# Kernel tuning notes

Hardware: AMD Instinct MI355X
Metric: run time of the kernel (lower is better)

The kernel has to match this reference:

```python
import jax, jax.numpy as jnp
import numpy as np

LN_EPS = 1e-12


def setup_inputs() -> dict:
    key = jax.random.key(0)
    ks = jax.random.split(key, 10)
    B, S, W, D, H = 16, 512, 5, 200, 768
    std = 0.02
    return {
        "layer_output": jax.random.normal(ks[0], (B, S, H), dtype=jnp.float32),
        "word_embeddings": jax.random.normal(ks[1], (B, S, W, D), dtype=jnp.float32),
        "word_mask": jax.random.randint(ks[2], (B, S, W), 0, 2, dtype=jnp.int64),
        "W1": jax.random.normal(ks[3], (D, H), dtype=jnp.float32) * std,
        "b1": jnp.zeros((H,), dtype=jnp.float32),
        "W2": jax.random.normal(ks[4], (H, H), dtype=jnp.float32) * std,
        "b2": jnp.zeros((H,), dtype=jnp.float32),
        "attn_W": jax.random.normal(ks[5], (H, H), dtype=jnp.float32) * std,
        "ln_gamma": jnp.ones((H,), dtype=jnp.float32),
        "ln_beta": jnp.zeros((H,), dtype=jnp.float32),
    }


def reference(layer_output, word_embeddings, word_mask, W1, b1, W2, b2, attn_W, ln_gamma, ln_beta):
    # word_transform: Linear -> Tanh -> Linear (dropout = identity in eval)
    we = jnp.tanh(jnp.einsum("bswd,dh->bswh", word_embeddings, W1) + b1)
    we = jnp.einsum("bswh,hk->bswk", we, W2) + b2  # [B,S,W,H]

    # bilinear word attention: (x @ attn_W) . word_outputs -> score over W
    q = jnp.einsum("bsh,hk->bsk", layer_output, attn_W)  # [B,S,H]
    alpha = jnp.einsum("bsk,bswk->bsw", q, we)            # [B,S,W]
    alpha = alpha + (1.0 - word_mask.astype(alpha.dtype)) * -10000.0
    alpha = jax.nn.softmax(alpha, axis=-1)

    # weighted sum over words + residual
    agg = jnp.einsum("bsw,bswh->bsh", alpha, we)
    h = layer_output + agg

    # LayerNorm (fuse_layer; dropout = identity in eval)
    mu = jnp.mean(h, axis=-1, keepdims=True)
    var = jnp.mean(jnp.square(h - mu), axis=-1, keepdims=True)
    return (h - mu) * jax.lax.rsqrt(var + LN_EPS) * ln_gamma + ln_beta
```

## Files before the change

### kernel.cpp

```cpp
#include <hip/hip_runtime.h>
#include <hip/hip_bf16.h>
#include <math.h>


typedef __attribute__((ext_vector_type(8))) short bf16x8;
typedef __attribute__((ext_vector_type(4))) float f32x4;

__device__ __forceinline__ unsigned short f2bf_bits(float f) {
    __hip_bfloat16 h = __float2bfloat16(f);
    return *reinterpret_cast<unsigned short*>(&h);
}
__device__ __forceinline__ float bf_bits2f(unsigned short u) {
    union { unsigned int i; float f; } v; v.i = ((unsigned int)u) << 16; return v.f;
}
__device__ __forceinline__ float tanh_fast(float x) {
    float xc = fminf(fmaxf(x, -9.f), 9.f);
    float t  = __expf(2.f * xc);
    return (t - 1.f) * __builtin_amdgcn_rcpf(t + 1.f);
}
__device__ __forceinline__ bf16x8 pack8(float4 a, float4 b) {
    union { bf16x8 v; unsigned short s[8]; } u;
    u.s[0]=f2bf_bits(a.x); u.s[1]=f2bf_bits(a.y); u.s[2]=f2bf_bits(a.z); u.s[3]=f2bf_bits(a.w);
    u.s[4]=f2bf_bits(b.x); u.s[5]=f2bf_bits(b.y); u.s[6]=f2bf_bits(b.z); u.s[7]=f2bf_bits(b.w);
    return u.v;
}

__device__ __forceinline__ void async_cp16(const void* g, void* lds) {
#if __has_builtin(__builtin_amdgcn_global_load_lds)
    auto gp = (const __attribute__((address_space(1))) unsigned int*)g;
    auto lp = (__attribute__((address_space(3))) unsigned int*)lds;
    __builtin_amdgcn_global_load_lds(gp, lp, 16, 0, 0);
#else
    *(uint4*)lds = *(const uint4*)g;
#endif
}

__device__ __forceinline__ void sched_fence()  { asm volatile("" ::: "memory"); }
__device__ __forceinline__ void wait8_barrier(){ asm volatile("s_waitcnt vmcnt(8)\ns_barrier" ::: "memory"); }
__device__ __forceinline__ void wait0_barrier(){ asm volatile("s_waitcnt vmcnt(0)\ns_barrier" ::: "memory"); }
__device__ __forceinline__ void barrier_only() { asm volatile("s_barrier" ::: "memory"); }

template<bool F32SRC, bool HAS_BIAS, bool TANH_ACT, bool RESID, bool OUT_BF16,
         int N, int K, int KREAL>
__device__ __forceinline__ void gemm_body(
    const void* __restrict__ Ap, const void* __restrict__ Btp,
    const float* __restrict__ bias, const float* __restrict__ resid,
    void* __restrict__ outp, int m0, int n0, unsigned char* smem)
{
    constexpr int NIT = K / 64;
    const int tid  = threadIdx.x;
    const int lane = tid & 63;
    const int wave = tid >> 6;
    const int wm   = wave & 1;
    const int wn   = wave >> 1;
    const int row16 = lane & 15;
    const int kq    = lane >> 4;

    f32x4 acc[4][4];
#pragma unroll
    for (int i = 0; i < 4; i++)
#pragma unroll
        for (int j = 0; j < 4; j++) acc[i][j] = (f32x4){0.f, 0.f, 0.f, 0.f};

    auto compute_tile = [&](const unsigned short* As, const unsigned short* Bs, bool full) {
        bf16x8 af[2][4], bg[2][4];
#pragma unroll
        for (int mi = 0; mi < 4; mi++) {
            const int r = wm * 64 + mi * 16 + row16;
            af[0][mi] = *(const bf16x8*)&As[r * 64 + (kq ^ (r & 7)) * 8];
            if (full) af[1][mi] = *(const bf16x8*)&As[r * 64 + ((4 + kq) ^ (r & 7)) * 8];
        }
#pragma unroll
        for (int ni = 0; ni < 4; ni++) {
            const int r = wn * 64 + ni * 16 + row16;
            bg[0][ni] = *(const bf16x8*)&Bs[r * 64 + (kq ^ (r & 7)) * 8];
            if (full) bg[1][ni] = *(const bf16x8*)&Bs[r * 64 + ((4 + kq) ^ (r & 7)) * 8];
        }
        __builtin_amdgcn_s_setprio(1);
#pragma unroll
        for (int mi = 0; mi < 4; mi++)
#pragma unroll
            for (int ni = 0; ni < 4; ni++)
                acc[mi][ni] = __builtin_amdgcn_mfma_f32_16x16x32_bf16(
                    af[0][mi], bg[0][ni], acc[mi][ni], 0, 0, 0);
        if (full) {
#pragma unroll
            for (int mi = 0; mi < 4; mi++)
#pragma unroll
                for (int ni = 0; ni < 4; ni++)
                    acc[mi][ni] = __builtin_amdgcn_mfma_f32_16x16x32_bf16(
                        af[1][mi], bg[1][ni], acc[mi][ni], 0, 0, 0);
        }
        __builtin_amdgcn_s_setprio(0);
    };

    if constexpr (F32SRC) {
        const float* A32 = (const float*)Ap;
        const float* B32 = (const float*)Btp;
        unsigned short* As = (unsigned short*)smem;
        unsigned short* Bs = As + 8192;
        for (int t = 0; t < NIT; ++t) {
#pragma unroll
            for (int i = 0; i < 4; ++i) {
                const int c = i * 256 + tid;
                const int row = c >> 3, sl = c & 7;
                const int kcc = sl ^ (row & 7);
                const float* sa = A32 + (size_t)(m0 + row) * K + t * 64 + kcc * 8;
                *(bf16x8*)&As[row * 64 + sl * 8] = pack8(*(const float4*)sa, *(const float4*)(sa + 4));
                const float* sb = B32 + (size_t)(n0 + row) * K + t * 64 + kcc * 8;
                *(bf16x8*)&Bs[row * 64 + sl * 8] = pack8(*(const float4*)sb, *(const float4*)(sb + 4));
            }
            __syncthreads();
            compute_tile(As, Bs, true);
            __syncthreads();
        }
    } else {
        const __hip_bfloat16* A  = (const __hip_bfloat16*)Ap;
        const __hip_bfloat16* Bt = (const __hip_bfloat16*)Btp;
        const int rsub = lane >> 3;
        const int slot = lane & 7;
        const int kc   = slot ^ rsub;
        const __hip_bfloat16* gA = A  + (size_t)(m0 + wave * 32 + rsub) * K + kc * 8;
        const __hip_bfloat16* gB = Bt + (size_t)(n0 + wave * 32 + rsub) * K + kc * 8;
        unsigned short* lA0 = (unsigned short*)smem + wave * 2048 + lane * 8;
        unsigned short* lB0 = lA0 + 8192;

        auto stage = [&](int t, int buf) {
            unsigned short* lA = lA0 + buf * 16384;
            unsigned short* lB = lB0 + buf * 16384;
            const __hip_bfloat16* a = gA + t * 64;
            const __hip_bfloat16* b = gB + t * 64;
#pragma unroll
            for (int i = 0; i < 4; i++) {
                async_cp16(a + (size_t)(8 * i) * K, lA + i * 512);
                async_cp16(b + (size_t)(8 * i) * K, lB + i * 512);
            }
            sched_fence();
        };

        stage(0, 0);
        if (NIT > 1) stage(1, 1);
#pragma unroll
        for (int t = 0; t < NIT; ++t) {
            if (t == NIT - 1) wait0_barrier(); else wait8_barrier();
            const unsigned short* As = (const unsigned short*)(smem + (t & 1) * 32768);
            const unsigned short* Bs = As + 8192;
            compute_tile(As, Bs, (t * 64 + 32 < KREAL));
            barrier_only();
            if (t + 2 < NIT) stage(t + 2, t & 1);
        }
    }

    if (OUT_BF16) {
        unsigned short* rep = (unsigned short*)smem;
#pragma unroll
        for (int ni = 0; ni < 4; ni++) {
            const int c = wn * 64 + ni * 16 + row16;
            float bcol = HAS_BIAS ? bias[n0 + c] : 0.f;
#pragma unroll
            for (int mi = 0; mi < 4; mi++)
#pragma unroll
                for (int r = 0; r < 4; r++) {
                    const int rr = wm * 64 + mi * 16 + kq * 4 + r;
                    float v = acc[mi][ni][r];
                    if (HAS_BIAS) v += bcol;
                    if (TANH_ACT) v = tanh_fast(v);
                    rep[rr * 132 + c] = f2bf_bits(v);
                }
        }
        __syncthreads();
#pragma unroll
        for (int p = 0; p < 8; p++) {
            const int lin = p * 256 + tid;
            const int row = lin >> 4;
            const int c8  = lin & 15;
            const unsigned short* s = &rep[row * 132 + c8 * 8];
            union { uint4 u; unsigned long long q[2]; } d;
            d.q[0] = *(const unsigned long long*)(s);
            d.q[1] = *(const unsigned long long*)(s + 4);
            *(uint4*)((__hip_bfloat16*)outp + (size_t)(m0 + row) * N + n0 + c8 * 8) = d.u;
        }
    } else {
        float* rep = (float*)smem;
#pragma unroll
        for (int h = 0; h < 2; h++) {
            if (wm == h) {
#pragma unroll
                for (int ni = 0; ni < 4; ni++) {
                    const int c = wn * 64 + ni * 16 + row16;
                    float bcol = HAS_BIAS ? bias[n0 + c] : 0.f;
#pragma unroll
                    for (int mi = 0; mi < 4; mi++)
#pragma unroll
                        for (int r = 0; r < 4; r++) {
                            const int rr = mi * 16 + kq * 4 + r;
                            float v = acc[mi][ni][r];
                            if (HAS_BIAS) v += bcol;
                            if (TANH_ACT) v = tanh_fast(v);
                            rep[rr * 132 + c] = v;
                        }
                }
            }
            __syncthreads();
#pragma unroll
            for (int p = 0; p < 8; p++) {
                const int lin = p * 256 + tid;
                const int row = lin >> 5;
                const int c4  = lin & 31;
                float4 v = *(const float4*)&rep[row * 132 + c4 * 4];
                const int grow = m0 + h * 64 + row;
                if (RESID) {
                    float4 rv = *(const float4*)&resid[(size_t)grow * N + n0 + c4 * 4];
                    v.x += rv.x; v.y += rv.y; v.z += rv.z; v.w += rv.w;
                }
                *(float4*)((float*)outp + (size_t)grow * N + n0 + c4 * 4) = v;
            }
            __syncthreads();
        }
    }
}

template<bool HAS_BIAS, bool TANH_ACT, bool RESID, bool OUT_BF16, int N, int K, int GX>
__global__ __launch_bounds__(256) void mfma_gemm(
    const __hip_bfloat16* __restrict__ A,
    const __hip_bfloat16* __restrict__ Bt,
    const float* __restrict__ bias,
    const float* __restrict__ resid,
    void* __restrict__ outp)
{
    __shared__ __align__(16) unsigned char smem[65536];
    int bx, by;
    {
        const int total = gridDim.x;
        const int per_xcd = total >> 3;
        if ((total & 7) == 0 && (per_xcd % GX) == 0) {
            int xcd = blockIdx.x & 7, idx = blockIdx.x >> 3;
            int lin = xcd * per_xcd + idx;
            by = lin / GX; bx = lin % GX;
        } else { by = blockIdx.x / GX; bx = blockIdx.x % GX; }
    }
    gemm_body<false, HAS_BIAS, TANH_ACT, RESID, OUT_BF16, N, K, K>(
        A, Bt, bias, resid, outp, by * 128, bx * 128, smem);
}

__global__ __launch_bounds__(256) void tgemm_kernel(
    const __hip_bfloat16* __restrict__ Eb,
    const __hip_bfloat16* __restrict__ W1Tb,
    const float* __restrict__ b1,
    __hip_bfloat16* __restrict__ Tb)
{
    __shared__ __align__(16) unsigned char smem[65536];
    const int xcd = blockIdx.x & 7, idx = blockIdx.x >> 3;
    const int lin = xcd * 240 + idx;
    gemm_body<false, true, true, false, true, 768, 256, 224>(
        Eb, W1Tb, b1, nullptr, Tb, (lin / 6) * 128, (lin % 6) * 128, smem);
}

__global__ __launch_bounds__(256) void prep_kernel(
    const float* __restrict__ x,  __hip_bfloat16* __restrict__ xb,
    const float* __restrict__ w2,
    const float* __restrict__ aw,
    const float* __restrict__ E,  __hip_bfloat16* __restrict__ Eb,
    const float* __restrict__ W1, __hip_bfloat16* __restrict__ W1Tb,
    __hip_bfloat16* __restrict__ W2Tb,
    __hip_bfloat16* __restrict__ Ctb)
{
    __shared__ __align__(16) unsigned char smem[33792];
    float (*tile)[33] = (float(*)[33])smem;
    const int b = blockIdx.x, tid = threadIdx.x;
    if (b < 36) {
        gemm_body<true, false, false, false, true, 768, 768, 768>(
            w2, aw, nullptr, nullptr, Ctb, (b / 6) * 128, (b % 6) * 128, smem);
    } else if (b < 804) {
        const float* in; __hip_bfloat16* outb; int R, C, Rpad, t;
        if (b < 228) { t = b - 36;  in = W1; outb = W1Tb; R = 200; C = 768; Rpad = 256; }
        else         { t = b - 228; in = w2; outb = W2Tb; R = 768; C = 768; Rpad = 768; }
        const int c0 = (t % 24) * 32, r0 = (t / 24) * 32;
        const int xx = tid & 31, yy = tid >> 5;
#pragma unroll
        for (int i = 0; i < 32; i += 8) {
            int r = r0 + yy + i;
            tile[yy + i][xx] = (r < R) ? in[(size_t)r * C + c0 + xx] : 0.f;
        }
        __syncthreads();
#pragma unroll
        for (int i = 0; i < 32; i += 8)
            outb[(size_t)(c0 + yy + i) * Rpad + r0 + xx] = __float2bfloat16(tile[xx][yy + i]);
    } else if (b < 1572) {
        const long long base = (long long)(b - 804) * 2048 + tid;
        float4 v[8];
#pragma unroll
        for (int j = 0; j < 8; j++) v[j] = ((const float4*)x)[base + j * 256];
#pragma unroll
        for (int j = 0; j < 8; j++)
            ((ushort4*)xb)[base + j * 256] =
                make_ushort4(f2bf_bits(v[j].x), f2bf_bits(v[j].y), f2bf_bits(v[j].z), f2bf_bits(v[j].w));
    } else {
        const int lane = tid & 63, wave = tid >> 6;
        const long long r0 = (long long)(b - 1572) * 32 + wave * 8;
        const int k = lane * 4;
        float4 v[8];
#pragma unroll
        for (int j = 0; j < 8; j++) {
            v[j] = make_float4(0.f, 0.f, 0.f, 0.f);
            if (k < 200) v[j] = *(const float4*)&E[(r0 + j) * 200 + k];
        }
#pragma unroll
        for (int j = 0; j < 8; j++)
            *(ushort4*)&Eb[(r0 + j) * 256 + k] =
                make_ushort4(f2bf_bits(v[j].x), f2bf_bits(v[j].y), f2bf_bits(v[j].z), f2bf_bits(v[j].w));
    }
}

__global__ __launch_bounds__(256) void attn_kernel(
    const __hip_bfloat16* __restrict__ T,
    const __hip_bfloat16* P,
    const int* __restrict__ mask,
    __hip_bfloat16* S)
{
    const int lane = threadIdx.x & 63;
    const int wave = threadIdx.x >> 6;
    const int r    = blockIdx.x * 4 + wave;
    const int base = lane * 12;

    float pv[12];
    {
        const ushort4* pp = (const ushort4*)((const unsigned short*)P + (size_t)r * 768 + base);
        ushort4 u0 = pp[0], u1 = pp[1], u2 = pp[2];
        unsigned short us[12] = {u0.x,u0.y,u0.z,u0.w, u1.x,u1.y,u1.z,u1.w, u2.x,u2.y,u2.z,u2.w};
#pragma unroll
        for (int j = 0; j < 12; j++) pv[j] = bf_bits2f(us[j]);
    }
    float tv[5][12], part[5];
#pragma unroll
    for (int w = 0; w < 5; w++) {
        const ushort4* tp = (const ushort4*)((const unsigned short*)T + ((size_t)r * 5 + w) * 768 + base);
        ushort4 u0 = tp[0], u1 = tp[1], u2 = tp[2];
        unsigned short us[12] = {u0.x,u0.y,u0.z,u0.w, u1.x,u1.y,u1.z,u1.w, u2.x,u2.y,u2.z,u2.w};
        float s = 0.f;
#pragma unroll
        for (int j = 0; j < 12; j++) { tv[w][j] = bf_bits2f(us[j]); s += tv[w][j] * pv[j]; }
        part[w] = s;
    }
#pragma unroll
    for (int off = 32; off > 0; off >>= 1)
#pragma unroll
        for (int w = 0; w < 5; w++)
            part[w] += __shfl_xor(part[w], off, 64);

    float logit[5], mx = -1e30f;
#pragma unroll
    for (int w = 0; w < 5; w++) {
        float m = (float)mask[(size_t)r * 5 + w];
        logit[w] = part[w] - 10000.0f * (1.0f - m);
        mx = fmaxf(mx, logit[w]);
    }
    float se = 0.f;
#pragma unroll
    for (int w = 0; w < 5; w++) { logit[w] = expf(logit[w] - mx); se += logit[w]; }
    const float inv = 1.0f / se;

    unsigned short os[12];
#pragma unroll
    for (int j = 0; j < 12; j++) {
        float s = 0.f;
#pragma unroll
        for (int w = 0; w < 5; w++) s += logit[w] * tv[w][j];
        os[j] = f2bf_bits(s * inv);
    }
    ushort4* sp = (ushort4*)((unsigned short*)S + (size_t)r * 768 + base);
    sp[0] = make_ushort4(os[0], os[1], os[2],  os[3]);
    sp[1] = make_ushort4(os[4], os[5], os[6],  os[7]);
    sp[2] = make_ushort4(os[8], os[9], os[10], os[11]);
}

__global__ __launch_bounds__(256) void ln_kernel(
    const float* __restrict__ Hbuf, const float* __restrict__ gamma,
    const float* __restrict__ beta, float* __restrict__ out)
{
    const int lane = threadIdx.x & 63;
    const int wave = threadIdx.x >> 6;
    const int r    = blockIdx.x * 4 + wave;
    const float* hr = Hbuf + (size_t)r * 768 + lane * 12;

    float v[12];
    {
        float4 a = *(const float4*)(hr);
        float4 b = *(const float4*)(hr + 4);
        float4 c = *(const float4*)(hr + 8);
        v[0]=a.x; v[1]=a.y; v[2]=a.z; v[3]=a.w;
        v[4]=b.x; v[5]=b.y; v[6]=b.z; v[7]=b.w;
        v[8]=c.x; v[9]=c.y; v[10]=c.z; v[11]=c.w;
    }
    float s = 0.f;
#pragma unroll
    for (int j = 0; j < 12; j++) s += v[j];
#pragma unroll
    for (int off = 32; off > 0; off >>= 1) s += __shfl_xor(s, off, 64);
    const float mu = s * (1.f / 768.f);
    float vs = 0.f;
#pragma unroll
    for (int j = 0; j < 12; j++) { float d = v[j] - mu; vs += d * d; }
#pragma unroll
    for (int off = 32; off > 0; off >>= 1) vs += __shfl_xor(vs, off, 64);
    const float rs = rsqrtf(vs * (1.f / 768.f) + 1e-12f);

    float o[12];
#pragma unroll
    for (int j = 0; j < 12; j++) {
        int h = lane * 12 + j;
        o[j] = (v[j] - mu) * rs * gamma[h] + beta[h];
    }
    float* orow = out + (size_t)r * 768 + lane * 12;
    *(float4*)(orow)     = make_float4(o[0], o[1], o[2],  o[3]);
    *(float4*)(orow + 4) = make_float4(o[4], o[5], o[6],  o[7]);
    *(float4*)(orow + 8) = make_float4(o[8], o[9], o[10], o[11]);
}

extern "C" void kernel_launch(void* const* d_in, const int* in_sizes, int n_in,
                              void* d_out, int out_size, void* d_ws, size_t ws_size,
                              hipStream_t stream)
{
    const float* x      = (const float*)d_in[0];
    const float* E      = (const float*)d_in[1];
    const int*   mask   = (const int*)d_in[2];
    const float* W1     = (const float*)d_in[3];
    const float* b1     = (const float*)d_in[4];
    const float* W2     = (const float*)d_in[5];
    const float* b2     = (const float*)d_in[6];
    const float* attn_W = (const float*)d_in[7];
    const float* gamma  = (const float*)d_in[8];
    const float* beta   = (const float*)d_in[9];
    float* out = (float*)d_out;

    const int BS = 8192, H = 768, M1 = 40960, KP = 256;

    char* p = (char*)d_ws;
    auto alloc = [&](size_t bytes) { char* q = p; p += (bytes + 255) & ~(size_t)255; return q; };
    __hip_bfloat16* xb    = (__hip_bfloat16*)alloc((size_t)BS * H * 2);
    __hip_bfloat16* W2Tb  = (__hip_bfloat16*)alloc((size_t)H * H * 2);
    __hip_bfloat16* Ctb   = (__hip_bfloat16*)alloc((size_t)H * H * 2);
    __hip_bfloat16* W1Tb  = (__hip_bfloat16*)alloc((size_t)H * KP * 2);
    __hip_bfloat16* Tb    = (__hip_bfloat16*)alloc((size_t)M1 * H * 2);
    __hip_bfloat16* Eb    = (__hip_bfloat16*)alloc((size_t)M1 * KP * 2);
    float* Hb = (float*)Tb;
    __hip_bfloat16* Pb = Eb;
    __hip_bfloat16* Sb = Pb;

    prep_kernel<<<2852, 256, 0, stream>>>(x, xb, W2, attn_W, E, Eb, W1, W1Tb, W2Tb, Ctb);

    tgemm_kernel<<<1920, 256, 0, stream>>>(Eb, W1Tb, b1, Tb);

    mfma_gemm<false, false, false, true, 768, 768, 6><<<384, 256, 0, stream>>>(
        xb, Ctb, nullptr, nullptr, Pb);

    attn_kernel<<<BS / 4, 256, 0, stream>>>(Tb, Pb, mask, Sb);

    mfma_gemm<true, false, true, false, 768, 768, 6><<<384, 256, 0, stream>>>(
        Sb, W2Tb, b2, x, Hb);

    ln_kernel<<<BS / 4, 256, 0, stream>>>(Hb, gamma, beta, out);
}
```

Baseline: 217.3 us.

## Make W1 GEMM persistent over five M-tiles with LDS-resident B and staged output

The tanh(E@W1+b1) GEMM kernel is rewritten so each block keeps the whole 128x256 W1 slice in LDS and walks five consecutive 128-row M tiles. A-tiles are double-buffered, and the last K step skips its padded half. Output goes through an LDS staging buffer so global stores are coalesced 16-byte writes. The grid drops from 1920 to 384 blocks. This removes repeated loading of B and per-block launch overhead, but 129 KB of LDS per block limits occupancy to one block per CU and leaves fewer blocks to spread across CUs.

```diff
diff --git a/kernel.cpp b/kernel.cpp
--- a/kernel.cpp
+++ b/kernel.cpp
@@ -37,8 +37,10 @@
 
 __device__ __forceinline__ void sched_fence()  { asm volatile("" ::: "memory"); }
 __device__ __forceinline__ void wait8_barrier(){ asm volatile("s_waitcnt vmcnt(8)\ns_barrier" ::: "memory"); }
+__device__ __forceinline__ void wait4_barrier(){ asm volatile("s_waitcnt vmcnt(4)\ns_barrier" ::: "memory"); }
 __device__ __forceinline__ void wait0_barrier(){ asm volatile("s_waitcnt vmcnt(0)\ns_barrier" ::: "memory"); }
 __device__ __forceinline__ void barrier_only() { asm volatile("s_barrier" ::: "memory"); }
+__device__ __forceinline__ void lgkm_barrier() { asm volatile("s_waitcnt lgkmcnt(0)\ns_barrier" ::: "memory"); }
 
 template<bool F32SRC, bool HAS_BIAS, bool TANH_ACT, bool RESID, bool OUT_BF16,
          int N, int K, int KREAL>
@@ -249,11 +251,127 @@
     const float* __restrict__ b1,
     __hip_bfloat16* __restrict__ Tb)
 {
-    __shared__ __align__(16) unsigned char smem[65536];
-    const int xcd = blockIdx.x & 7, idx = blockIdx.x >> 3;
-    const int lin = xcd * 240 + idx;
-    gemm_body<false, true, true, false, true, 768, 256, 224>(
-        Eb, W1Tb, b1, nullptr, Tb, (lin / 6) * 128, (lin % 6) * 128, smem);
+    __shared__ __align__(16) unsigned char smem[132096];
+    unsigned short* Bs_all = (unsigned short*)smem;
+    unsigned short* As_all = (unsigned short*)(smem + 65536);
+    unsigned short* rep    = (unsigned short*)(smem + 98304);
+
+    const int tid  = threadIdx.x;
+    const int lane = tid & 63;
+    const int wave = tid >> 6;
+    const int wm   = wave & 1;
+    const int wn   = wave >> 1;
+    const int row16 = lane & 15;
+    const int kq    = lane >> 4;
+
+    const int lin = (blockIdx.x & 7) * 48 + (blockIdx.x >> 3);
+    const int mg  = lin / 6;
+    const int bx  = lin % 6;
+
+#pragma unroll
+    for (int kt = 0; kt < 4; ++kt)
+#pragma unroll
+        for (int i = 0; i < 4; ++i) {
+            const int c = i * 256 + tid;
+            const int row = c >> 3, sl = c & 7;
+            const int kcc = sl ^ (row & 7);
+            async_cp16(W1Tb + (size_t)(bx * 128 + row) * 256 + kt * 64 + kcc * 8,
+                       Bs_all + kt * 8192 + c * 8);
+        }
+    sched_fence();
+
+    auto stageA = [&](int mt, int t, int buf) {
+        const int m0 = mg * 640 + mt * 128;
+#pragma unroll
+        for (int i = 0; i < 4; ++i) {
+            const int c = i * 256 + tid;
+            const int row = c >> 3, sl = c & 7;
+            const int kcc = sl ^ (row & 7);
+            async_cp16(Eb + (size_t)(m0 + row) * 256 + t * 64 + kcc * 8,
+                       As_all + buf * 8192 + c * 8);
+        }
+        sched_fence();
+    };
+
+    stageA(0, 0, 0);
+    stageA(0, 1, 1);
+
+    for (int mt = 0; mt < 5; ++mt) {
+        f32x4 acc[4][4];
+#pragma unroll
+        for (int i = 0; i < 4; i++)
+#pragma unroll
+            for (int j = 0; j < 4; j++) acc[i][j] = (f32x4){0.f, 0.f, 0.f, 0.f};
+
+#pragma unroll
+        for (int t = 0; t < 4; ++t) {
+            const int idx = mt * 4 + t;
+            if (idx == 19) wait0_barrier(); else wait4_barrier();
+
+            const unsigned short* As = As_all + (idx & 1) * 8192;
+            const unsigned short* Bs = Bs_all + t * 8192;
+            const bool full = (t < 3);
+
+            bf16x8 af[2][4], bg[2][4];
+#pragma unroll
+            for (int mi = 0; mi < 4; mi++) {
+                const int r = wm * 64 + mi * 16 + row16;
+                af[0][mi] = *(const bf16x8*)&As[r * 64 + (kq ^ (r & 7)) * 8];
+                if (full) af[1][mi] = *(const bf16x8*)&As[r * 64 + ((4 + kq) ^ (r & 7)) * 8];
+            }
+#pragma unroll
+            for (int ni = 0; ni < 4; ni++) {
+                const int r = wn * 64 + ni * 16 + row16;
+                bg[0][ni] = *(const bf16x8*)&Bs[r * 64 + (kq ^ (r & 7)) * 8];
+                if (full) bg[1][ni] = *(const bf16x8*)&Bs[r * 64 + ((4 + kq) ^ (r & 7)) * 8];
+            }
+            __builtin_amdgcn_s_setprio(1);
+#pragma unroll
+            for (int mi = 0; mi < 4; mi++)
+#pragma unroll
+                for (int ni = 0; ni < 4; ni++)
+                    acc[mi][ni] = __builtin_amdgcn_mfma_f32_16x16x32_bf16(
+                        af[0][mi], bg[0][ni], acc[mi][ni], 0, 0, 0);
+            if (full) {
+#pragma unroll
+                for (int mi = 0; mi < 4; mi++)
+#pragma unroll
+                    for (int ni = 0; ni < 4; ni++)
+                        acc[mi][ni] = __builtin_amdgcn_mfma_f32_16x16x32_bf16(
+                            af[1][mi], bg[1][ni], acc[mi][ni], 0, 0, 0);
+            }
+            __builtin_amdgcn_s_setprio(0);
+            barrier_only();
+            if (idx + 2 < 20) stageA((idx + 2) >> 2, (idx + 2) & 3, idx & 1);
+        }
+
+        const int m0 = mg * 640 + mt * 128;
+#pragma unroll
+        for (int ni = 0; ni < 4; ni++) {
+            const int c = wn * 64 + ni * 16 + row16;
+            const float bcol = b1[bx * 128 + c];
+#pragma unroll
+            for (int mi = 0; mi < 4; mi++)
+#pragma unroll
+                for (int r = 0; r < 4; r++) {
+                    const int rr = wm * 64 + mi * 16 + kq * 4 + r;
+                    rep[rr * 132 + c] = f2bf_bits(tanh_fast(acc[mi][ni][r] + bcol));
+                }
+        }
+        lgkm_barrier();
+#pragma unroll
+        for (int p = 0; p < 8; p++) {
+            const int linc = p * 256 + tid;
+            const int row = linc >> 4;
+            const int c8  = linc & 15;
+            const unsigned short* s = &rep[row * 132 + c8 * 8];
+            union { uint4 u; unsigned long long q[2]; } d;
+            d.q[0] = *(const unsigned long long*)(s);
+            d.q[1] = *(const unsigned long long*)(s + 4);
+            *(uint4*)(Tb + (size_t)(m0 + row) * 768 + bx * 128 + c8 * 8) = d.u;
+        }
+        if (mt < 4) barrier_only();
+    }
 }
 
 __global__ __launch_bounds__(256) void prep_kernel(
@@ -449,7 +567,7 @@
 
     prep_kernel<<<2852, 256, 0, stream>>>(x, xb, W2, attn_W, E, Eb, W1, W1Tb, W2Tb, Ctb);
 
-    tgemm_kernel<<<1920, 256, 0, stream>>>(Eb, W1Tb, b1, Tb);
+    tgemm_kernel<<<384, 256, 0, stream>>>(Eb, W1Tb, b1, Tb);
 
     mfma_gemm<false, false, false, true, 768, 768, 6><<<384, 256, 0, stream>>>(
         xb, Ctb, nullptr, nullptr, Pb);
```

Measured after the change: 244.5 us. 12.5% more time.
